# Kernel optimization log

Measured on AMD Instinct MI355X. Metric: run time of the kernel, lower is better.

## Reference

```python
import jax, jax.numpy as jnp
import numpy as np

NUM_HEADS = 16
HEAD_DIM = 128
RMS_EPS = 1e-6


def _rms_norm(x):
    # RMSNorm over last dim, no learned weight
    return x * jax.lax.rsqrt(jnp.mean(jnp.square(x), axis=-1, keepdims=True) + RMS_EPS)


def _rotary_cos_sin(T, head_dim, dtype=jnp.float32):
    # half-truncated RoPE: quarter of dims get frequencies, next quarter gets freq 0
    dim_quarter = max(1, head_dim // 4)
    angular_freq = (1.0 / 1024.0) ** jnp.linspace(0.0, 1.0, dim_quarter, dtype=dtype)
    angular_freq = jnp.concatenate([angular_freq, jnp.zeros(dim_quarter, dtype=dtype)])  # [head_dim//2]
    t = jnp.arange(T, dtype=dtype)
    theta = t[:, None] * angular_freq[None, :]  # [T, head_dim//2]
    return jnp.cos(theta), jnp.sin(theta)


def _apply_rotary(x_BTHD, cos, sin):
    # x: [B,T,H,D]; cos/sin: [T, D//2]
    c = cos[None, :, None, :]
    s = sin[None, :, None, :]
    x1, x2 = jnp.split(x_BTHD, 2, axis=-1)
    y1 = x1 * c + x2 * s
    y2 = -x1 * s + x2 * c
    return jnp.concatenate([y1, y2], axis=-1)


def setup_inputs() -> dict:
    key = jax.random.key(0)
    k1, k2, k3 = jax.random.split(key, 3)
    B, T, dim = 1, 2048, 2048
    hdim = NUM_HEADS * HEAD_DIM
    std = 0.5 * dim ** (-0.5)
    x = jax.random.normal(k1, (B, T, dim), dtype=jnp.float32)
    Wqkv = jax.random.normal(k2, (3, hdim, dim), dtype=jnp.float32) * std
    Wout = jax.random.normal(k3, (dim, hdim), dtype=jnp.float32) * std
    return {"x": x, "Wqkv": Wqkv, "Wout": Wout}


def reference(x, Wqkv, Wout):
    B, T, dim = x.shape
    H, D = NUM_HEADS, HEAD_DIM
    scale = 1.0 / (D ** 0.5)

    # fused QKV projection: [B,T,3,H,D]
    qkv = jnp.einsum('btd,ehd->bteh'.replace('eh', 'f'), x, Wqkv.reshape(3 * H * D, dim))  # [B,T,3HD]
    qkv = qkv.reshape(B, T, 3, H, D)
    q, k, v = qkv[:, :, 0], qkv[:, :, 1], qkv[:, :, 2]  # each [B,T,H,D]

    q, k = _rms_norm(q), _rms_norm(k)
    cos, sin = _rotary_cos_sin(T, D, dtype=jnp.float32)
    q, k = _apply_rotary(q, cos, sin), _apply_rotary(k, cos, sin)

    # causal attention
    scores = jnp.einsum('bthd,bshd->bhts', q, k) * scale  # [B,H,T,T]
    causal = jnp.tril(jnp.ones((T, T), dtype=bool))
    scores = jnp.where(causal[None, None], scores, -jnp.inf)
    probs = jax.nn.softmax(scores, axis=-1)
    y = jnp.einsum('bhts,bshd->bthd', probs, v)  # [B,T,H,D]

    y = y.reshape(B, T, H * D)
    return y @ Wout.T
```

## Files before the change

kernel.cpp:

```cpp
#include <hip/hip_runtime.h>
#include <hip/hip_bf16.h>
#include <stdint.h>

typedef __hip_bfloat16 bf16;
typedef __bf16 bf16x8 __attribute__((ext_vector_type(8)));
typedef float f32x4 __attribute__((ext_vector_type(4)));

#define MFMA16(a, b, c) __builtin_amdgcn_mfma_f32_16x16x32_bf16((a), (b), (c), 0, 0, 0)

__device__ __forceinline__ void gload_lds16(const void* g, void* l) {
    __builtin_amdgcn_global_load_lds((const __attribute__((address_space(1))) void*)g,
                                     (__attribute__((address_space(3))) void*)l, 16, 0, 0);
}

struct alignas(16) B8 { bf16 v[8]; };
struct alignas(8)  B4 { bf16 v[4]; };

__global__ __launch_bounds__(256) void cast_all_k(
    const float* __restrict__ x, const float* __restrict__ wqkv, const float* __restrict__ wout,
    bf16* __restrict__ xb, bf16* __restrict__ wqkvb, bf16* __restrict__ woutb) {
    const size_t NX = (size_t)2048 * 2048 / 8;
    const size_t NW = (size_t)3 * 2048 * 2048 / 8;
    size_t i = (size_t)blockIdx.x * 256 + threadIdx.x;
    const float* s; bf16* d;
    if (i < NX)            { s = x;    d = xb; }
    else if (i < NX + NW)  { s = wqkv; d = wqkvb; i -= NX; }
    else                   { s = wout; d = woutb; i -= NX + NW; }
    float4 a = ((const float4*)s)[2 * i];
    float4 b = ((const float4*)s)[2 * i + 1];
    B8 t;
    t.v[0] = __float2bfloat16(a.x); t.v[1] = __float2bfloat16(a.y);
    t.v[2] = __float2bfloat16(a.z); t.v[3] = __float2bfloat16(a.w);
    t.v[4] = __float2bfloat16(b.x); t.v[5] = __float2bfloat16(b.y);
    t.v[6] = __float2bfloat16(b.z); t.v[7] = __float2bfloat16(b.w);
    ((B8*)d)[i] = t;
}

__global__ __launch_bounds__(256) void gemm_bt(
    const bf16* __restrict__ A, const bf16* __restrict__ B, float* __restrict__ C,
    int M, int N, int K) {
    __shared__ __align__(16) bf16 As[2][128 * 32];
    __shared__ __align__(16) bf16 Bs[2][128 * 32];
    const int t = threadIdx.x;
    const int lane = t & 63, w = t >> 6;
    const int wr = w >> 1, wc = w & 1;
    const int l15 = lane & 15, lg = lane >> 4;
    const int m0 = blockIdx.y * 128, n0 = blockIdx.x * 128;

    const int row = t >> 2, cb = t & 3;
    const int row1 = (t + 256) >> 2, cb1 = t & 3;

    f32x4 acc[4][4] = {};

#define G_STAGE(buf, k0)                                                        \
    do {                                                                        \
        gload_lds16(&A[(size_t)(m0 + row) * K + (k0) + cb * 8],                 \
                    &As[buf][t * 8]);                                           \
        gload_lds16(&B[(size_t)(n0 + row) * K + (k0) + cb * 8],                 \
                    &Bs[buf][t * 8]);                                           \
        gload_lds16(&A[(size_t)(m0 + row1) * K + (k0) + cb1 * 8],               \
                    &As[buf][(t + 256) * 8]);                                   \
        gload_lds16(&B[(size_t)(n0 + row1) * K + (k0) + cb1 * 8],               \
                    &Bs[buf][(t + 256) * 8]);                                   \
    } while (0)

    G_STAGE(0, 0);
    int cur = 0;
    for (int k0 = 0; k0 < K; k0 += 32) {
        const bool hn = (k0 + 32 < K);
        if (hn) {
            G_STAGE(cur ^ 1, k0 + 32);
            asm volatile("s_waitcnt vmcnt(4)" ::: "memory");
        } else {
            asm volatile("s_waitcnt vmcnt(0)" ::: "memory");
        }
        __builtin_amdgcn_s_barrier();
        __builtin_amdgcn_sched_barrier(0);

        bf16x8 af[4], bfr[4];
#pragma unroll
        for (int mi = 0; mi < 4; ++mi)
            af[mi] = *(const bf16x8*)&As[cur][(wr * 64 + mi * 16 + l15) * 32 + lg * 8];
#pragma unroll
        for (int ni = 0; ni < 4; ++ni)
            bfr[ni] = *(const bf16x8*)&Bs[cur][(wc * 64 + ni * 16 + l15) * 32 + lg * 8];
#pragma unroll
        for (int mi = 0; mi < 4; ++mi)
#pragma unroll
            for (int ni = 0; ni < 4; ++ni)
                acc[mi][ni] = MFMA16(af[mi], bfr[ni], acc[mi][ni]);
        __builtin_amdgcn_s_barrier();
        cur ^= 1;
    }
#undef G_STAGE

#pragma unroll
    for (int mi = 0; mi < 4; ++mi) {
        int r0 = m0 + wr * 64 + mi * 16 + lg * 4;
#pragma unroll
        for (int ni = 0; ni < 4; ++ni) {
            int c0 = n0 + wc * 64 + ni * 16 + l15;
#pragma unroll
            for (int j = 0; j < 4; ++j)
                C[(size_t)(r0 + j) * N + c0] = acc[mi][ni][j];
        }
    }
}

__global__ __launch_bounds__(128) void normrope_k(
    const float* __restrict__ qkv, bf16* __restrict__ qb, bf16* __restrict__ kb) {
    const int t = blockIdx.x, h = blockIdx.y, d = threadIdx.x;
    const float* base = qkv + (size_t)t * 6144;
    float q = base[h * 128 + d];
    float k = base[2048 + h * 128 + d];

    __shared__ float red[4];
    __shared__ float qn[128], kn[128];
    float sq = q * q, sk = k * k;
#pragma unroll
    for (int m = 1; m <= 32; m <<= 1) {
        sq += __shfl_xor(sq, m);
        sk += __shfl_xor(sk, m);
    }
    if ((d & 63) == 0) { red[(d >> 6) * 2] = sq; red[(d >> 6) * 2 + 1] = sk; }
    __syncthreads();
    float rq = rsqrtf((red[0] + red[2]) * (1.0f / 128.0f) + 1e-6f);
    float rk = rsqrtf((red[1] + red[3]) * (1.0f / 128.0f) + 1e-6f);
    qn[d] = q * rq;
    kn[d] = k * rk;
    __syncthreads();

    int j = d & 63;
    float c = 1.0f, s = 0.0f;
    if (j < 32) {
        float af = exp2f(-10.0f * (float)j / 31.0f);
        float theta = (float)t * af;
        sincosf(theta, &s, &c);
    }
    float oq, ok;
    if (d < 64) { oq =  qn[d] * c + qn[d + 64] * s;  ok =  kn[d] * c + kn[d + 64] * s; }
    else        { oq = -qn[d - 64] * s + qn[d] * c;  ok = -kn[d - 64] * s + kn[d] * c; }

    size_t oidx = ((size_t)h * 2048 + t) * 128 + d;
    qb[oidx] = __float2bfloat16(oq * 0.08838834764831845f);
    kb[oidx] = __float2bfloat16(ok);
}

__global__ __launch_bounds__(256) void vtrans_k(
    const float* __restrict__ qkv, bf16* __restrict__ vt) {
    __shared__ bf16 Ts[64][72];
    const int t0 = blockIdx.x * 64, d0 = blockIdx.y * 64, h = blockIdx.z;
    const int tid = threadIdx.x;
#pragma unroll
    for (int it = 0; it < 4; ++it) {
        int f = tid + it * 256;
        int tl = f >> 4, dl = (f & 15) * 4;
        float4 v = *(const float4*)&qkv[(size_t)(t0 + tl) * 6144 + 4096 + h * 128 + d0 + dl];
        Ts[tl][dl + 0] = __float2bfloat16(v.x);
        Ts[tl][dl + 1] = __float2bfloat16(v.y);
        Ts[tl][dl + 2] = __float2bfloat16(v.z);
        Ts[tl][dl + 3] = __float2bfloat16(v.w);
    }
    __syncthreads();
#pragma unroll
    for (int it = 0; it < 2; ++it) {
        int f = tid + it * 256;
        int dl = f >> 3, tc = f & 7;
        B8 p;
#pragma unroll
        for (int i = 0; i < 8; ++i) p.v[i] = Ts[tc * 8 + i][dl];
        *(B8*)&vt[((size_t)h * 128 + d0 + dl) * 2048 + t0 + tc * 8] = p;
    }
}

__global__ __launch_bounds__(256) void attn_main_k(
    const bf16* __restrict__ qg, const bf16* __restrict__ kg,
    const bf16* __restrict__ vt, float* __restrict__ part) {
    const int T = 2048, D = 128;
    const int cz = blockIdx.x, qt = blockIdx.y, h = blockIdx.z;
    if (cz > (qt >> 3)) return;
    const int qb0 = qt * 64;
    const int kstart = cz * 512;
    const int kend = min(kstart + 512, (qt + 1) * 64);

    __shared__ __align__(16) bf16 Ks[2][64 * 128];
    __shared__ __align__(16) bf16 Vs[2][64 * 128];
    __shared__ __align__(16) bf16 Ps[4][16 * 64];

    const int t = threadIdx.x;
    const int lane = t & 63, w = t >> 6;
    const int l15 = lane & 15, lg = lane >> 4;

    const size_t qoff = ((size_t)h * T + qb0 + w * 16 + l15) * D;
    bf16x8 qf[4];
#pragma unroll
    for (int ks = 0; ks < 4; ++ks)
        qf[ks] = *(const bf16x8*)&qg[qoff + ks * 32 + lg * 8];

    f32x4 o[8] = {};
    float mrow[4] = {-1e30f, -1e30f, -1e30f, -1e30f};
    float lrow[4] = {0.f, 0.f, 0.f, 0.f};

#define A_STAGE(buf, k0)                                                         \
    do {                                                                         \
        _Pragma("unroll")                                                        \
        for (int c = 0; c < 4; ++c) {                                            \
            int f = t + c * 256;                                                 \
            int krow = f >> 4, kc = f & 15;                                      \
            gload_lds16(&kg[((size_t)h * T + (k0) + krow) * D + ((kc ^ (krow & 15)) * 8)], \
                        &Ks[buf][f * 8]);                                        \
            int dr = f >> 3, vc = f & 7;                                         \
            gload_lds16(&vt[((size_t)h * D + dr) * T + (k0) + ((vc ^ (dr & 7)) * 8)],      \
                        &Vs[buf][f * 8]);                                        \
        }                                                                        \
    } while (0)

    A_STAGE(0, kstart);
    int cur = 0;
    for (int k0 = kstart; k0 < kend; k0 += 64) {
        const bool hn = (k0 + 64 < kend);
        if (hn) {
            A_STAGE(cur ^ 1, k0 + 64);
            asm volatile("s_waitcnt vmcnt(8)" ::: "memory");
        } else {
            asm volatile("s_waitcnt vmcnt(0)" ::: "memory");
        }
        __builtin_amdgcn_s_barrier();
        __builtin_amdgcn_sched_barrier(0);

        f32x4 sc[4] = {};
#pragma unroll
        for (int ks = 0; ks < 4; ++ks) {
#pragma unroll
            for (int nb = 0; nb < 4; ++nb) {
                int key = nb * 16 + l15;
                int c = ks * 4 + lg;
                bf16x8 kf = *(const bf16x8*)&Ks[cur][key * 128 + ((c ^ (key & 15)) * 8)];
                sc[nb] = MFMA16(qf[ks], kf, sc[nb]);
            }
        }

        const bool diag = (k0 == qb0);
        const int qrow_base = qb0 + w * 16 + lg * 4;
#pragma unroll
        for (int j = 0; j < 4; ++j) {
            float s0 = sc[0][j], s1 = sc[1][j], s2 = sc[2][j], s3 = sc[3][j];
            if (diag) {
                int qrow = qrow_base + j;
                if (k0 + l15 > qrow)      s0 = -1e30f;
                if (k0 + 16 + l15 > qrow) s1 = -1e30f;
                if (k0 + 32 + l15 > qrow) s2 = -1e30f;
                if (k0 + 48 + l15 > qrow) s3 = -1e30f;
            }
            float tm = fmaxf(fmaxf(s0, s1), fmaxf(s2, s3));
            tm = fmaxf(tm, __shfl_xor(tm, 1));
            tm = fmaxf(tm, __shfl_xor(tm, 2));
            tm = fmaxf(tm, __shfl_xor(tm, 4));
            tm = fmaxf(tm, __shfl_xor(tm, 8));
            float mnew = fmaxf(mrow[j], tm);
            float fac = __expf(mrow[j] - mnew);
            float p0 = __expf(s0 - mnew), p1 = __expf(s1 - mnew);
            float p2 = __expf(s2 - mnew), p3 = __expf(s3 - mnew);
            float ps = (p0 + p1) + (p2 + p3);
            ps += __shfl_xor(ps, 1);
            ps += __shfl_xor(ps, 2);
            ps += __shfl_xor(ps, 4);
            ps += __shfl_xor(ps, 8);
            lrow[j] = lrow[j] * fac + ps;
            mrow[j] = mnew;
#pragma unroll
            for (int nd = 0; nd < 8; ++nd) o[nd][j] *= fac;
            int prow = lg * 4 + j;
            int sub = l15 & 7, hi = l15 >> 3;
            bf16* pw = &Ps[w][prow * 64 + sub];
            pw[(((0 + hi) ^ (prow & 7)) * 8)] = __float2bfloat16(p0);
            pw[(((2 + hi) ^ (prow & 7)) * 8)] = __float2bfloat16(p1);
            pw[(((4 + hi) ^ (prow & 7)) * 8)] = __float2bfloat16(p2);
            pw[(((6 + hi) ^ (prow & 7)) * 8)] = __float2bfloat16(p3);
        }

#pragma unroll
        for (int hk = 0; hk < 2; ++hk) {
            bf16x8 pf = *(const bf16x8*)&Ps[w][l15 * 64 + (((hk * 4 + lg) ^ (l15 & 7)) * 8)];
#pragma unroll
            for (int nd = 0; nd < 8; ++nd) {
                int dd = nd * 16 + l15;
                bf16x8 vf = *(const bf16x8*)&Vs[cur][dd * 64 + (((hk * 4 + lg) ^ (dd & 7)) * 8)];
                o[nd] = MFMA16(pf, vf, o[nd]);
            }
        }
        __builtin_amdgcn_s_barrier();
        cur ^= 1;
    }
#undef A_STAGE

    int b = qt >> 3, rr = qt & 7;
    int slot = h * 80 + qt + 4 * b * (b - 1) + rr * b + cz;
    float* rec = part + (size_t)slot * 8320;
    if (l15 == 0) {
#pragma unroll
        for (int j = 0; j < 4; ++j) {
            rec[w * 16 + lg * 4 + j] = mrow[j];
            rec[64 + w * 16 + lg * 4 + j] = lrow[j];
        }
    }
#pragma unroll
    for (int nd = 0; nd < 8; ++nd)
#pragma unroll
        for (int j = 0; j < 4; ++j)
            rec[128 + (w * 16 + lg * 4 + j) * 128 + nd * 16 + l15] = o[nd][j];
}

__global__ __launch_bounds__(256) void attn_merge_k(
    const float* __restrict__ part, bf16* __restrict__ y) {
    const int qt = blockIdx.x, h = blockIdx.y, tid = threadIdx.x;
    const int nch = (qt >> 3) + 1;
    int b = qt >> 3, rr = qt & 7;
    const int base = h * 80 + qt + 4 * b * (b - 1) + rr * b;
    const int r = tid >> 2;
    const int d0 = (tid & 3) * 32;

    float mi[4], li[4], wgt[4];
    float M = -1e30f;
#pragma unroll
    for (int i = 0; i < 4; ++i) {
        if (i < nch) {
            mi[i] = part[(size_t)(base + i) * 8320 + r];
            li[i] = part[(size_t)(base + i) * 8320 + 64 + r];
            M = fmaxf(M, mi[i]);
        } else { mi[i] = -1e30f; li[i] = 0.f; }
    }
    float L = 0.f;
#pragma unroll
    for (int i = 0; i < 4; ++i) {
        wgt[i] = (i < nch) ? __expf(mi[i] - M) : 0.f;
        L += li[i] * wgt[i];
    }
    float invL = 1.0f / L;

    bf16* yrow = &y[(size_t)(qt * 64 + r) * 2048 + h * 128 + d0];
#pragma unroll
    for (int dd = 0; dd < 32; dd += 4) {
        float a0 = 0.f, a1 = 0.f, a2 = 0.f, a3 = 0.f;
#pragma unroll
        for (int i = 0; i < 4; ++i) {
            if (i < nch) {
                const float4 ov = *(const float4*)&part[(size_t)(base + i) * 8320 + 128 + r * 128 + d0 + dd];
                a0 += wgt[i] * ov.x; a1 += wgt[i] * ov.y;
                a2 += wgt[i] * ov.z; a3 += wgt[i] * ov.w;
            }
        }
        B4 p;
        p.v[0] = __float2bfloat16(a0 * invL);
        p.v[1] = __float2bfloat16(a1 * invL);
        p.v[2] = __float2bfloat16(a2 * invL);
        p.v[3] = __float2bfloat16(a3 * invL);
        *(B4*)&yrow[dd] = p;
    }
}

extern "C" void kernel_launch(void* const* d_in, const int* in_sizes, int n_in,
                              void* d_out, int out_size, void* d_ws, size_t ws_size,
                              hipStream_t stream) {
    const float* x    = (const float*)d_in[0];
    const float* wqkv = (const float*)d_in[1];
    const float* wout = (const float*)d_in[2];
    float* out = (float*)d_out;

    char* ws = (char*)d_ws;
    bf16*  xb    = (bf16*)(ws);
    bf16*  wqkvb = (bf16*)(ws + 8388608);
    bf16*  woutb = (bf16*)(ws + 33554432);
    float* qkvf  = (float*)(ws + 41943040);
    bf16*  qb    = (bf16*)(ws + 92274688);
    bf16*  kb    = (bf16*)(ws + 100663296);
    bf16*  vt    = (bf16*)(ws + 109051904);
    bf16*  yb    = (bf16*)(ws + 117440512);

    cast_all_k<<<10240, 256, 0, stream>>>(x, wqkv, wout, xb, wqkvb, woutb);
    gemm_bt<<<dim3(48, 16), 256, 0, stream>>>(xb, wqkvb, qkvf, 2048, 6144, 2048);
    normrope_k<<<dim3(2048, 16), 128, 0, stream>>>(qkvf, qb, kb);
    vtrans_k<<<dim3(32, 2, 16), 256, 0, stream>>>(qkvf, vt);
    attn_main_k<<<dim3(4, 32, 16), 256, 0, stream>>>(qb, kb, vt, qkvf);
    attn_merge_k<<<dim3(32, 16), 256, 0, stream>>>(qkvf, yb);
    gemm_bt<<<dim3(16, 16), 256, 0, stream>>>(yb, woutb, out, 2048, 2048, 2048);
}
```

Measured before the change: 371.8 us.

## Split attention into finer key chunks with lazy rescale and bf16 partials

Attention splits the key range into 256-key chunks instead of 512, which doubles the number of split blocks for more parallelism. The double-buffered async K/V staging is replaced by a single buffer with sync, which frees LDS for occupancy. The online softmax skips rescaling while the new max stays within a threshold, and row sums are computed by an MFMA against a ones vector instead of shuffles. Partial outputs are stored as bf16 to halve merge traffic. The trade-offs are loss of load/compute overlap, more partials to merge, and extra precision loss from the bf16 partials and the lazy max.

```diff
diff --git a/kernel.cpp b/kernel.cpp
--- a/kernel.cpp
+++ b/kernel.cpp
@@ -175,16 +175,16 @@
 
 __global__ __launch_bounds__(256) void attn_main_k(
     const bf16* __restrict__ qg, const bf16* __restrict__ kg,
-    const bf16* __restrict__ vt, float* __restrict__ part) {
+    const bf16* __restrict__ vt, char* __restrict__ part) {
     const int T = 2048, D = 128;
     const int cz = blockIdx.x, qt = blockIdx.y, h = blockIdx.z;
-    if (cz > (qt >> 3)) return;
+    if (cz > (qt >> 2)) return;
     const int qb0 = qt * 64;
-    const int kstart = cz * 512;
-    const int kend = min(kstart + 512, (qt + 1) * 64);
-
-    __shared__ __align__(16) bf16 Ks[2][64 * 128];
-    __shared__ __align__(16) bf16 Vs[2][64 * 128];
+    const int kstart = cz * 256;
+    const int kend = min(kstart + 256, (qt + 1) * 64);
+
+    __shared__ __align__(16) bf16 Ks[64 * 128];
+    __shared__ __align__(16) bf16 Vs[128 * 64];
     __shared__ __align__(16) bf16 Ps[4][16 * 64];
 
     const int t = threadIdx.x;
@@ -197,36 +197,26 @@
     for (int ks = 0; ks < 4; ++ks)
         qf[ks] = *(const bf16x8*)&qg[qoff + ks * 32 + lg * 8];
 
+    bf16x8 onesf;
+#pragma unroll
+    for (int i = 0; i < 8; ++i) onesf[i] = (__bf16)1.0f;
+
     f32x4 o[8] = {};
     float mrow[4] = {-1e30f, -1e30f, -1e30f, -1e30f};
     float lrow[4] = {0.f, 0.f, 0.f, 0.f};
 
-#define A_STAGE(buf, k0)                                                         \
-    do {                                                                         \
-        _Pragma("unroll")                                                        \
-        for (int c = 0; c < 4; ++c) {                                            \
-            int f = t + c * 256;                                                 \
-            int krow = f >> 4, kc = f & 15;                                      \
-            gload_lds16(&kg[((size_t)h * T + (k0) + krow) * D + ((kc ^ (krow & 15)) * 8)], \
-                        &Ks[buf][f * 8]);                                        \
-            int dr = f >> 3, vc = f & 7;                                         \
-            gload_lds16(&vt[((size_t)h * D + dr) * T + (k0) + ((vc ^ (dr & 7)) * 8)],      \
-                        &Vs[buf][f * 8]);                                        \
-        }                                                                        \
-    } while (0)
-
-    A_STAGE(0, kstart);
-    int cur = 0;
     for (int k0 = kstart; k0 < kend; k0 += 64) {
-        const bool hn = (k0 + 64 < kend);
-        if (hn) {
-            A_STAGE(cur ^ 1, k0 + 64);
-            asm volatile("s_waitcnt vmcnt(8)" ::: "memory");
-        } else {
-            asm volatile("s_waitcnt vmcnt(0)" ::: "memory");
-        }
-        __builtin_amdgcn_s_barrier();
-        __builtin_amdgcn_sched_barrier(0);
+#pragma unroll
+        for (int c = 0; c < 4; ++c) {
+            int f = t + c * 256;
+            int krow = f >> 4, kc = f & 15;
+            gload_lds16(&kg[((size_t)h * T + k0 + krow) * D + ((kc ^ (krow & 15)) * 8)],
+                        &Ks[f * 8]);
+            int dr = f >> 3, vc = f & 7;
+            gload_lds16(&vt[((size_t)h * D + dr) * T + k0 + ((vc ^ (dr & 7)) * 8)],
+                        &Vs[f * 8]);
+        }
+        __syncthreads();
 
         f32x4 sc[4] = {};
 #pragma unroll
@@ -235,13 +225,15 @@
             for (int nb = 0; nb < 4; ++nb) {
                 int key = nb * 16 + l15;
                 int c = ks * 4 + lg;
-                bf16x8 kf = *(const bf16x8*)&Ks[cur][key * 128 + ((c ^ (key & 15)) * 8)];
+                bf16x8 kf = *(const bf16x8*)&Ks[key * 128 + ((c ^ (key & 15)) * 8)];
                 sc[nb] = MFMA16(qf[ks], kf, sc[nb]);
             }
         }
 
         const bool diag = (k0 == qb0);
         const int qrow_base = qb0 + w * 16 + lg * 4;
+        float fac[4];
+        bool anyresc = false;
 #pragma unroll
         for (int j = 0; j < 4; ++j) {
             float s0 = sc[0][j], s1 = sc[1][j], s2 = sc[2][j], s3 = sc[3][j];
@@ -257,19 +249,16 @@
             tm = fmaxf(tm, __shfl_xor(tm, 2));
             tm = fmaxf(tm, __shfl_xor(tm, 4));
             tm = fmaxf(tm, __shfl_xor(tm, 8));
-            float mnew = fmaxf(mrow[j], tm);
-            float fac = __expf(mrow[j] - mnew);
-            float p0 = __expf(s0 - mnew), p1 = __expf(s1 - mnew);
-            float p2 = __expf(s2 - mnew), p3 = __expf(s3 - mnew);
-            float ps = (p0 + p1) + (p2 + p3);
-            ps += __shfl_xor(ps, 1);
-            ps += __shfl_xor(ps, 2);
-            ps += __shfl_xor(ps, 4);
-            ps += __shfl_xor(ps, 8);
-            lrow[j] = lrow[j] * fac + ps;
-            mrow[j] = mnew;
-#pragma unroll
-            for (int nd = 0; nd < 8; ++nd) o[nd][j] *= fac;
+            if (__all(tm <= mrow[j] + 6.0f)) {
+                fac[j] = 1.0f;
+            } else {
+                float mnew = fmaxf(mrow[j], tm);
+                fac[j] = __expf(mrow[j] - mnew);
+                mrow[j] = mnew;
+                anyresc = true;
+            }
+            float p0 = __expf(s0 - mrow[j]), p1 = __expf(s1 - mrow[j]);
+            float p2 = __expf(s2 - mrow[j]), p3 = __expf(s3 - mrow[j]);
             int prow = lg * 4 + j;
             int sub = l15 & 7, hi = l15 >> 3;
             bf16* pw = &Ps[w][prow * 64 + sub];
@@ -279,60 +268,73 @@
             pw[(((6 + hi) ^ (prow & 7)) * 8)] = __float2bfloat16(p3);
         }
 
+        if (anyresc) {
+#pragma unroll
+            for (int nd = 0; nd < 8; ++nd)
+#pragma unroll
+                for (int j = 0; j < 4; ++j) o[nd][j] *= fac[j];
+        }
+
+        f32x4 lsum = {};
 #pragma unroll
         for (int hk = 0; hk < 2; ++hk) {
             bf16x8 pf = *(const bf16x8*)&Ps[w][l15 * 64 + (((hk * 4 + lg) ^ (l15 & 7)) * 8)];
+            lsum = MFMA16(pf, onesf, lsum);
 #pragma unroll
             for (int nd = 0; nd < 8; ++nd) {
                 int dd = nd * 16 + l15;
-                bf16x8 vf = *(const bf16x8*)&Vs[cur][dd * 64 + (((hk * 4 + lg) ^ (dd & 7)) * 8)];
+                bf16x8 vf = *(const bf16x8*)&Vs[dd * 64 + (((hk * 4 + lg) ^ (dd & 7)) * 8)];
                 o[nd] = MFMA16(pf, vf, o[nd]);
             }
         }
-        __builtin_amdgcn_s_barrier();
-        cur ^= 1;
-    }
-#undef A_STAGE
-
-    int b = qt >> 3, rr = qt & 7;
-    int slot = h * 80 + qt + 4 * b * (b - 1) + rr * b + cz;
-    float* rec = part + (size_t)slot * 8320;
+#pragma unroll
+        for (int j = 0; j < 4; ++j) lrow[j] = lrow[j] * fac[j] + lsum[j];
+        __syncthreads();
+    }
+
+    int B = qt >> 2, r4 = qt & 3;
+    int slot = h * 144 + qt + 2 * B * (B - 1) + r4 * B + cz;
+    char* rec = part + (size_t)slot * 16896;
+    float* mrec = (float*)rec;
+    float* lrec = (float*)(rec + 256);
+    bf16*  orec = (bf16*)(rec + 512);
     if (l15 == 0) {
 #pragma unroll
         for (int j = 0; j < 4; ++j) {
-            rec[w * 16 + lg * 4 + j] = mrow[j];
-            rec[64 + w * 16 + lg * 4 + j] = lrow[j];
+            mrec[w * 16 + lg * 4 + j] = mrow[j];
+            lrec[w * 16 + lg * 4 + j] = lrow[j];
         }
     }
 #pragma unroll
     for (int nd = 0; nd < 8; ++nd)
 #pragma unroll
         for (int j = 0; j < 4; ++j)
-            rec[128 + (w * 16 + lg * 4 + j) * 128 + nd * 16 + l15] = o[nd][j];
+            orec[(w * 16 + lg * 4 + j) * 128 + nd * 16 + l15] = __float2bfloat16(o[nd][j]);
 }
 
 __global__ __launch_bounds__(256) void attn_merge_k(
-    const float* __restrict__ part, bf16* __restrict__ y) {
+    const char* __restrict__ part, bf16* __restrict__ y) {
     const int qt = blockIdx.x, h = blockIdx.y, tid = threadIdx.x;
-    const int nch = (qt >> 3) + 1;
-    int b = qt >> 3, rr = qt & 7;
-    const int base = h * 80 + qt + 4 * b * (b - 1) + rr * b;
+    const int nch = (qt >> 2) + 1;
+    int B = qt >> 2, r4 = qt & 3;
+    const int base = h * 144 + qt + 2 * B * (B - 1) + r4 * B;
     const int r = tid >> 2;
     const int d0 = (tid & 3) * 32;
 
-    float mi[4], li[4], wgt[4];
+    float mi[8], li[8], wgt[8];
     float M = -1e30f;
 #pragma unroll
-    for (int i = 0; i < 4; ++i) {
+    for (int i = 0; i < 8; ++i) {
         if (i < nch) {
-            mi[i] = part[(size_t)(base + i) * 8320 + r];
-            li[i] = part[(size_t)(base + i) * 8320 + 64 + r];
+            const char* rec = part + (size_t)(base + i) * 16896;
+            mi[i] = ((const float*)rec)[r];
+            li[i] = ((const float*)(rec + 256))[r];
             M = fmaxf(M, mi[i]);
         } else { mi[i] = -1e30f; li[i] = 0.f; }
     }
     float L = 0.f;
 #pragma unroll
-    for (int i = 0; i < 4; ++i) {
+    for (int i = 0; i < 8; ++i) {
         wgt[i] = (i < nch) ? __expf(mi[i] - M) : 0.f;
         L += li[i] * wgt[i];
     }
@@ -340,22 +342,22 @@
 
     bf16* yrow = &y[(size_t)(qt * 64 + r) * 2048 + h * 128 + d0];
 #pragma unroll
-    for (int dd = 0; dd < 32; dd += 4) {
-        float a0 = 0.f, a1 = 0.f, a2 = 0.f, a3 = 0.f;
-#pragma unroll
-        for (int i = 0; i < 4; ++i) {
+    for (int dd = 0; dd < 32; dd += 8) {
+        float facc[8] = {};
+#pragma unroll
+        for (int i = 0; i < 8; ++i) {
             if (i < nch) {
-                const float4 ov = *(const float4*)&part[(size_t)(base + i) * 8320 + 128 + r * 128 + d0 + dd];
-                a0 += wgt[i] * ov.x; a1 += wgt[i] * ov.y;
-                a2 += wgt[i] * ov.z; a3 += wgt[i] * ov.w;
-            }
-        }
-        B4 p;
-        p.v[0] = __float2bfloat16(a0 * invL);
-        p.v[1] = __float2bfloat16(a1 * invL);
-        p.v[2] = __float2bfloat16(a2 * invL);
-        p.v[3] = __float2bfloat16(a3 * invL);
-        *(B4*)&yrow[dd] = p;
+                const bf16* orec = (const bf16*)(part + (size_t)(base + i) * 16896 + 512);
+                B8 ov = *(const B8*)&orec[r * 128 + d0 + dd];
+#pragma unroll
+                for (int e = 0; e < 8; ++e)
+                    facc[e] += wgt[i] * __bfloat162float(ov.v[e]);
+            }
+        }
+        B8 p;
+#pragma unroll
+        for (int e = 0; e < 8; ++e) p.v[e] = __float2bfloat16(facc[e] * invL);
+        *(B8*)&yrow[dd] = p;
     }
 }
 
@@ -381,7 +383,7 @@
     gemm_bt<<<dim3(48, 16), 256, 0, stream>>>(xb, wqkvb, qkvf, 2048, 6144, 2048);
     normrope_k<<<dim3(2048, 16), 128, 0, stream>>>(qkvf, qb, kb);
     vtrans_k<<<dim3(32, 2, 16), 256, 0, stream>>>(qkvf, vt);
-    attn_main_k<<<dim3(4, 32, 16), 256, 0, stream>>>(qb, kb, vt, qkvf);
-    attn_merge_k<<<dim3(32, 16), 256, 0, stream>>>(qkvf, yb);
+    attn_main_k<<<dim3(8, 32, 16), 256, 0, stream>>>(qb, kb, vt, (char*)qkvf);
+    attn_merge_k<<<dim3(32, 16), 256, 0, stream>>>((const char*)qkvf, yb);
     gemm_bt<<<dim3(16, 16), 256, 0, stream>>>(yb, woutb, out, 2048, 2048, 2048);
 }
```

Measured after the change: 355.7 us. -4.3%, faster.
